# Performance work log

Measured on AMD Instinct MI355X. Metric: run time of the kernel, lower is better.

The kernel has to match this reference:

```python
import jax, jax.numpy as jnp
import numpy as np

B, T, D, U, C = 256, 512, 128, 128, 64


def setup_inputs() -> dict:
    key = jax.random.key(0)
    ks = jax.random.split(key, 4)
    s_in = 1.0 / np.sqrt(D)
    s_u = 1.0 / np.sqrt(U)
    return {
        "inputs": jax.random.normal(ks[0], (B, T, D), dtype=jnp.float32),
        "W1": jax.random.normal(ks[1], (D, U), dtype=jnp.float32) * s_in,
        "b1": jnp.zeros((U,), dtype=jnp.float32),
        "W2": jax.random.normal(ks[2], (U, U), dtype=jnp.float32) * s_u,
        "b2": jnp.zeros((U,), dtype=jnp.float32),
        "Wc": jax.random.normal(ks[3], (U, C), dtype=jnp.float32) * s_u,
        "bc": jnp.zeros((C,), dtype=jnp.float32),
    }


def reference(inputs, W1, b1, W2, b2, Wc, bc):
    # state_{t} = tanh(x_t @ W1 + b1) + tanh(state_{t-1} @ W2 + b2)
    # Input projection has no recurrent dependency -> precompute in one big GEMM.
    h = jnp.tanh(jnp.einsum("btd,du->btu", inputs, W1) + b1)  # (B, T, U)

    def step(state, h_t):
        y = h_t + jnp.tanh(state @ W2 + b2)  # (B, U)
        return y, y

    state0 = jnp.zeros((inputs.shape[0], W2.shape[0]), dtype=inputs.dtype)
    _, ys = jax.lax.scan(step, state0, jnp.swapaxes(h, 0, 1))  # ys: (T, B, U)
    features = jnp.swapaxes(ys, 0, 1)  # (B, T, U)
    # classifier: Dense head applied to stacked features
    return jnp.einsum("btu,uc->btc", features, Wc) + bc
```

## Files before the change

### kernel.cpp

```cpp
#include <hip/hip_runtime.h>

#define NB 256
#define NT 512
#define ND 128
#define NU 128
#define NC 64
#define NM (NB * NT)
#define YP 136
#define SCL 2.8853900817779268f

typedef _Float16 half2v __attribute__((ext_vector_type(2)));
typedef _Float16 half4v __attribute__((ext_vector_type(4)));
typedef _Float16 half8v __attribute__((ext_vector_type(8)));
typedef float f32x4 __attribute__((ext_vector_type(4)));
typedef float v2f __attribute__((ext_vector_type(2)));

#define MFMA(a, b, c) __builtin_amdgcn_mfma_f32_16x16x32_f16((a), (b), (c), 0, 0, 0)

__device__ __forceinline__ half2v pk2(float a, float b) {
  return __builtin_bit_cast(half2v, __builtin_amdgcn_cvt_pkrtz(a, b));
}

__device__ __forceinline__ float tanh_s(float s) {
  float e = __builtin_amdgcn_exp2f(s);
  return fmaf(-2.0f, __builtin_amdgcn_rcpf(e + 1.0f), 1.0f);
}
__device__ __forceinline__ float ytanh(float s, float u) {
  float e = __builtin_amdgcn_exp2f(s);
  return fmaf(-2.0f, __builtin_amdgcn_rcpf(e + 1.0f), u);
}

__device__ __forceinline__ void wg_barrier() {
  asm volatile("s_waitcnt lgkmcnt(0)\n\ts_barrier" ::: "memory");
}

__global__ __launch_bounds__(256, 1) void k1_inproj(
    const float* __restrict__ x, const float* __restrict__ W1,
    const float* __restrict__ b1v, _Float16* __restrict__ TH)
{
  __shared__ _Float16 W1T[ND * YP];
  const int tid = (int)threadIdx.x;
  for (int i = tid; i < ND * NU / 2; i += 256) {
    int n = i & 127, kh = i >> 7;
    half2v p = {(_Float16)(SCL * W1[(size_t)(2 * kh) * NU + n]),
                (_Float16)(SCL * W1[(size_t)(2 * kh + 1) * NU + n])};
    *(half2v*)&W1T[n * YP + 2 * kh] = p;
  }
  __syncthreads();

  const int L = tid & 63, wv = tid >> 6;
  const int v = L & 15, q = L >> 4;
  const int m0 = (int)blockIdx.x * 64 + wv * 16;

  const float* xr = x + (size_t)(m0 + v) * ND + 8 * q;
  half8v xf[4];
#pragma unroll
  for (int kk = 0; kk < 4; ++kk) {
    float4 a = *(const float4*)(xr + 32 * kk);
    float4 b = *(const float4*)(xr + 32 * kk + 4);
    half2v p0 = pk2(a.x, a.y), p1 = pk2(a.z, a.w);
    half2v p2 = pk2(b.x, b.y), p3 = pk2(b.z, b.w);
    xf[kk] = (half8v){p0[0], p0[1], p1[0], p1[1], p2[0], p2[1], p3[0], p3[1]};
  }

#pragma unroll
  for (int ht = 0; ht < 8; ++ht) {
    f32x4 acc;
    {
      float4 bb = *(const float4*)&b1v[16 * ht + 4 * q];
      acc = (f32x4){SCL * bb.x, SCL * bb.y, SCL * bb.z, SCL * bb.w};
    }
#pragma unroll
    for (int kk = 0; kk < 4; ++kk) {
      half8v wa = *(const half8v*)&W1T[(16 * ht + v) * YP + 32 * kk + 8 * q];
      acc = MFMA(wa, xf[kk], acc);
    }
    half2v zlo = pk2(tanh_s(acc[0]), tanh_s(acc[1]));
    half2v zhi = pk2(tanh_s(acc[2]), tanh_s(acc[3]));
    half4v z = {zlo[0], zlo[1], zhi[0], zhi[1]};
    *(half4v*)&TH[(size_t)(m0 + v) * NU + 16 * ht + 4 * q] = z;
  }
}

__global__ __launch_bounds__(512, 1) void k2_recur(
    const _Float16* __restrict__ TH, const float* __restrict__ W2,
    const float* __restrict__ b2v, const float* __restrict__ Wc,
    const float* __restrict__ bcv, float* __restrict__ out)
{
  __shared__ _Float16 Ybuf[2][16 * YP];

  const int tid = (int)threadIdx.x;
  const int w = tid >> 6;
  const int L = tid & 63;
  const int v = L & 15, q = L >> 4;
  const int b0 = (int)blockIdx.x * 16;

  half8v w2f[4];
#pragma unroll
  for (int kk = 0; kk < 4; ++kk) {
    half8v h;
#pragma unroll
    for (int j = 0; j < 8; ++j)
      h[j] = (_Float16)(SCL * W2[(size_t)(32 * kk + 8 * q + j) * NU + 16 * w + v]);
    w2f[kk] = h;
  }
  f32x4 b2f;
  {
    float4 bb = *(const float4*)&b2v[16 * w + 4 * q];
    b2f = (f32x4){SCL * bb.x, SCL * bb.y, SCL * bb.z, SCL * bb.w};
  }

  const bool whead = (w < 4);
  half8v wcf[4];
  f32x4 bcf = (f32x4){0.f, 0.f, 0.f, 0.f};
  float* op = out;
  if (whead) {
#pragma unroll
    for (int kk = 0; kk < 4; ++kk) {
      half8v h;
#pragma unroll
      for (int j = 0; j < 8; ++j)
        h[j] = (_Float16)Wc[(size_t)(32 * kk + 8 * q + j) * NC + 16 * w + v];
      wcf[kk] = h;
    }
    float4 bb = *(const float4*)&bcv[16 * w + 4 * q];
    bcf = (f32x4){bb.x, bb.y, bb.z, bb.w};
    op = out + (size_t)(b0 + v) * NT * NC + 16 * w + 4 * q;
  }

  const _Float16* thp = TH + (size_t)(b0 + v) * NT * NU + 16 * w + 4 * q;

#define CVTU(A)                                                               \
  (f32x4){1.f + (float)(A)[0], 1.f + (float)(A)[1],                           \
          1.f + (float)(A)[2], 1.f + (float)(A)[3]}

  f32x4 uf0, uf1, uf2, uf3;
  {
    half4v a0 = *(const half4v*)(thp + 0 * NU);
    half4v a1 = *(const half4v*)(thp + 1 * NU);
    half4v a2 = *(const half4v*)(thp + 2 * NU);
    half4v a3 = *(const half4v*)(thp + 3 * NU);
    uf0 = CVTU(a0); uf1 = CVTU(a1); uf2 = CVTU(a2); uf3 = CVTU(a3);
  }
  half4v thr0 = *(const half4v*)(thp + 4 * NU);
  half4v thr1 = *(const half4v*)(thp + 5 * NU);
  half4v thr2 = *(const half4v*)(thp + 6 * NU);
  half4v thr3 = *(const half4v*)(thp + 7 * NU);

  f32x4 racc = b2f;
  _Float16* wr = &Ybuf[0][0] + v * YP + 16 * w + 4 * q;
  const _Float16* rd = &Ybuf[0][0] + v * YP + 8 * q;
  const f32x4 zero4 = (f32x4){0.f, 0.f, 0.f, 0.f};

#define K2STEP(T_, UF_, THR_, BUF_)                                           \
  {                                                                           \
    const int t_ = (T_);                                                      \
    half2v ylo = pk2(ytanh(racc[0], UF_[0]), ytanh(racc[1], UF_[1]));         \
    half2v yhi = pk2(ytanh(racc[2], UF_[2]), ytanh(racc[3], UF_[3]));         \
    half4v y4 = {ylo[0], ylo[1], yhi[0], yhi[1]};                             \
    *(half4v*)(wr + (BUF_) * (16 * YP)) = y4;                                 \
    wg_barrier();                                                             \
    half8v yf0 = *(const half8v*)(rd + (BUF_) * (16 * YP) + 0);               \
    half8v yf1 = *(const half8v*)(rd + (BUF_) * (16 * YP) + 32);              \
    half8v yf2 = *(const half8v*)(rd + (BUF_) * (16 * YP) + 64);              \
    half8v yf3 = *(const half8v*)(rd + (BUF_) * (16 * YP) + 96);              \
    f32x4 ra = MFMA(w2f[0], yf0, b2f);          \
    f32x4 rb = MFMA(w2f[1], yf1, zero4);                                      \
    ra = MFMA(w2f[2], yf2, ra);                                               \
    rb = MFMA(w2f[3], yf3, rb);                                               \
    if (whead) {                                                              \
      f32x4 oacc = bcf;                                                       \
      oacc = MFMA(wcf[0], yf0, oacc);                                         \
      oacc = MFMA(wcf[1], yf1, oacc);                                         \
      oacc = MFMA(wcf[2], yf2, oacc);                                         \
      oacc = MFMA(wcf[3], yf3, oacc);                                         \
      *(float4*)(op + (size_t)t_ * NC) =                                      \
          (float4){oacc[0], oacc[1], oacc[2], oacc[3]};                       \
    }                                                                         \
    {                                                                         \
      UF_ = CVTU(THR_);      \
      int tn = t_ + 8; tn = tn < NT ? tn : NT - 1;                            \
      THR_ = *(const half4v*)(thp + (size_t)tn * NU);                         \
    }                                                                         \
    racc = ra + rb;                                                           \
  }

#pragma unroll 1
  for (int t = 0; t < NT; t += 4) {
    K2STEP(t + 0, uf0, thr0, 0)
    K2STEP(t + 1, uf1, thr1, 1)
    K2STEP(t + 2, uf2, thr2, 0)
    K2STEP(t + 3, uf3, thr3, 1)
  }
#undef K2STEP
#undef CVTU
}

__device__ __forceinline__ float fast_tanh(float x) {
  float e = __expf(2.0f * x);
  return 1.0f - 2.0f / (e + 1.0f);
}
__device__ __forceinline__ float bcast(float val, int i) {
  return __builtin_bit_cast(float, __builtin_amdgcn_readlane(__builtin_bit_cast(int, val), i));
}

__global__ __launch_bounds__(256, 1) void rnn_fallback(
    const float* __restrict__ x, const float* __restrict__ W1,
    const float* __restrict__ b1v, const float* __restrict__ W2,
    const float* __restrict__ b2v, const float* __restrict__ Wc,
    const float* __restrict__ bcv, float* __restrict__ out)
{
  __shared__ float xring[16][ND];
  __shared__ float pH[2][4][NU];
  __shared__ float pR[2][4][NU];
  __shared__ float pC[2][4][NC];

  const int tid  = (int)threadIdx.x;
  const int lane = tid & 63;
  const int kg   = tid >> 6;
  const int b    = (int)blockIdx.x;
  const float4* xr4 = (const float4*)(x + (size_t)b * NT * ND);

  v2f w1f[32], w2f[32];
  float wcf[32];
#pragma unroll
  for (int i = 0; i < 32; ++i) {
    int k = kg * 32 + i;
    w1f[i] = (v2f){W1[k * NU + lane], W1[k * NU + lane + 64]};
    w2f[i] = (v2f){W2[k * NU + lane], W2[k * NU + lane + 64]};
    wcf[i] = Wc[k * NC + lane];
  }
  const float biasc = bcv[lane];
  float bias1 = 0.f, bias2 = 0.f;
  if (lane < 32) { bias1 = b1v[kg * 32 + lane]; bias2 = b2v[kg * 32 + lane]; }

  float4 stg = make_float4(0.f, 0.f, 0.f, 0.f);
  if (lane < 32) {
    float4 a0 = xr4[(kg + 0) * 32 + lane];
    float4 a1 = xr4[(kg + 4) * 32 + lane];
    ((float4*)xring[kg + 0])[lane] = a0;
    ((float4*)xring[kg + 4])[lane] = a1;
    stg = xr4[(kg + 8) * 32 + lane];
  }
  float yseg = 0.f;
  wg_barrier();

  for (int t = 0; t < NT; ++t) {
    const int pb = t & 1;
    v2f accH0 = {0.f, 0.f}, accH1 = {0.f, 0.f};
    const float4* xb = (const float4*)&xring[t & 15][kg * 32];
#pragma unroll
    for (int i = 0; i < 4; ++i) {
      float4 xa = xb[2 * i];
      float4 xc = xb[2 * i + 1];
      accH0 = w1f[8*i+0] * (v2f){xa.x, xa.x} + accH0;
      accH1 = w1f[8*i+1] * (v2f){xa.y, xa.y} + accH1;
      accH0 = w1f[8*i+2] * (v2f){xa.z, xa.z} + accH0;
      accH1 = w1f[8*i+3] * (v2f){xa.w, xa.w} + accH1;
      accH0 = w1f[8*i+4] * (v2f){xc.x, xc.x} + accH0;
      accH1 = w1f[8*i+5] * (v2f){xc.y, xc.y} + accH1;
      accH0 = w1f[8*i+6] * (v2f){xc.z, xc.z} + accH0;
      accH1 = w1f[8*i+7] * (v2f){xc.w, xc.w} + accH1;
    }
    v2f accH = accH0 + accH1;
    v2f accR0 = {0.f, 0.f}, accR1 = {0.f, 0.f};
    float accC0 = 0.f, accC1 = 0.f;
#pragma unroll
    for (int i = 0; i < 16; ++i) {
      float s0 = bcast(yseg, 2 * i);
      float s1 = bcast(yseg, 2 * i + 1);
      accR0 = w2f[2*i+0] * (v2f){s0, s0} + accR0;
      accR1 = w2f[2*i+1] * (v2f){s1, s1} + accR1;
      accC0 = fmaf(s0, wcf[2*i+0], accC0);
      accC1 = fmaf(s1, wcf[2*i+1], accC1);
    }
    v2f accR = accR0 + accR1;
    float accC = accC0 + accC1;

    pH[pb][kg][lane]      = accH.x;
    pH[pb][kg][lane + 64] = accH.y;
    pR[pb][kg][lane]      = accR.x;
    pR[pb][kg][lane + 64] = accR.y;
    pC[pb][kg][lane]      = accC;

    if (kg == (t & 3)) {
      if (lane < 32) {
        ((float4*)xring[(t + 8) & 15])[lane] = stg;
        int r = t + 12; r = (r < NT) ? r : (NT - 1);
        stg = xr4[r * 32 + lane];
      }
    }
    wg_barrier();
    if (lane < 32) {
      const int j = kg * 32 + lane;
      float hs = bias1, rs = bias2;
#pragma unroll
      for (int g = 0; g < 4; ++g) { hs += pH[pb][g][j]; rs += pR[pb][g][j]; }
      yseg = fast_tanh(hs) + fast_tanh(rs);
    }
    if (kg == ((t + 2) & 3) && t >= 1) {
      float cs = biasc;
#pragma unroll
      for (int g = 0; g < 4; ++g) cs += pC[pb][g][lane];
      out[((size_t)b * NT + (t - 1)) * NC + lane] = cs;
    }
  }
  float accC0 = 0.f, accC1 = 0.f;
#pragma unroll
  for (int i = 0; i < 16; ++i) {
    float s0 = bcast(yseg, 2 * i);
    float s1 = bcast(yseg, 2 * i + 1);
    accC0 = fmaf(s0, wcf[2*i+0], accC0);
    accC1 = fmaf(s1, wcf[2*i+1], accC1);
  }
  pC[0][kg][lane] = accC0 + accC1;
  wg_barrier();
  if (kg == 0) {
    float cs = biasc;
#pragma unroll
    for (int g = 0; g < 4; ++g) cs += pC[0][g][lane];
    out[((size_t)b * NT + (NT - 1)) * NC + lane] = cs;
  }
}

extern "C" void kernel_launch(void* const* d_in, const int* in_sizes, int n_in,
                              void* d_out, int out_size, void* d_ws, size_t ws_size,
                              hipStream_t stream) {
  (void)in_sizes; (void)n_in; (void)out_size;
  const float* x   = (const float*)d_in[0];
  const float* W1  = (const float*)d_in[1];
  const float* b1v = (const float*)d_in[2];
  const float* W2  = (const float*)d_in[3];
  const float* b2v = (const float*)d_in[4];
  const float* Wc  = (const float*)d_in[5];
  const float* bcv = (const float*)d_in[6];
  float* out = (float*)d_out;

  const size_t need = (size_t)NM * NU * 2;
  if (ws_size >= need) {
    _Float16* TH = (_Float16*)d_ws;
    hipLaunchKernelGGL(k1_inproj, dim3(NM / 64), dim3(256), 0, stream, x, W1, b1v, TH);
    hipLaunchKernelGGL(k2_recur, dim3(NB / 16), dim3(512), 0, stream,
                       TH, W2, b2v, Wc, bcv, out);
  } else {
    hipLaunchKernelGGL(rnn_fallback, dim3(NB), dim3(256), 0, stream,
                       x, W1, b1v, W2, b2v, Wc, bcv, out);
  }
}
```

Measured before the change: 318.5 us.

## Repartition recurrent kernel into two recurrence waves and one dedicated head wave

The recurrent kernel drops from eight waves to three. Two waves each own 64 hidden units and run the W2 recurrence; a third wave computes the whole 64-class classifier head from the shared y buffer. The state is now stored as y minus one, and the column sums of W2 and Wc are folded into the biases, which removes the per-step 1+th conversion. The aim is cheaper per-step workgroup barriers and less idle head work, at the cost of four times more MFMA and tanh work per recurrence wave on the serial critical path.

```diff
diff --git a/kernel.cpp b/kernel.cpp
--- a/kernel.cpp
+++ b/kernel.cpp
@@ -25,9 +25,9 @@
   float e = __builtin_amdgcn_exp2f(s);
   return fmaf(-2.0f, __builtin_amdgcn_rcpf(e + 1.0f), 1.0f);
 }
-__device__ __forceinline__ float ytanh(float s, float u) {
+__device__ __forceinline__ float ym1(float s, float th) {
   float e = __builtin_amdgcn_exp2f(s);
-  return fmaf(-2.0f, __builtin_amdgcn_rcpf(e + 1.0f), u);
+  return fmaf(-2.0f, __builtin_amdgcn_rcpf(e + 1.0f), th);
 }
 
 __device__ __forceinline__ void wg_barrier() {
@@ -82,7 +82,7 @@
   }
 }
 
-__global__ __launch_bounds__(512, 1) void k2_recur(
+__global__ __launch_bounds__(192, 1) void k2_recur(
     const _Float16* __restrict__ TH, const float* __restrict__ W2,
     const float* __restrict__ b2v, const float* __restrict__ Wc,
     const float* __restrict__ bcv, float* __restrict__ out)
@@ -94,106 +94,148 @@
   const int L = tid & 63;
   const int v = L & 15, q = L >> 4;
   const int b0 = (int)blockIdx.x * 16;
-
-  half8v w2f[4];
-#pragma unroll
-  for (int kk = 0; kk < 4; ++kk) {
-    half8v h;
-#pragma unroll
-    for (int j = 0; j < 8; ++j)
-      h[j] = (_Float16)(SCL * W2[(size_t)(32 * kk + 8 * q + j) * NU + 16 * w + v]);
-    w2f[kk] = h;
-  }
-  f32x4 b2f;
-  {
-    float4 bb = *(const float4*)&b2v[16 * w + 4 * q];
-    b2f = (f32x4){SCL * bb.x, SCL * bb.y, SCL * bb.z, SCL * bb.w};
-  }
-
-  const bool whead = (w < 4);
-  half8v wcf[4];
-  f32x4 bcf = (f32x4){0.f, 0.f, 0.f, 0.f};
-  float* op = out;
-  if (whead) {
-#pragma unroll
-    for (int kk = 0; kk < 4; ++kk) {
-      half8v h;
-#pragma unroll
-      for (int j = 0; j < 8; ++j)
-        h[j] = (_Float16)Wc[(size_t)(32 * kk + 8 * q + j) * NC + 16 * w + v];
-      wcf[kk] = h;
-    }
-    float4 bb = *(const float4*)&bcv[16 * w + 4 * q];
-    bcf = (f32x4){bb.x, bb.y, bb.z, bb.w};
-    op = out + (size_t)(b0 + v) * NT * NC + 16 * w + 4 * q;
-  }
-
-  const _Float16* thp = TH + (size_t)(b0 + v) * NT * NU + 16 * w + 4 * q;
-
-#define CVTU(A)                                                               \
-  (f32x4){1.f + (float)(A)[0], 1.f + (float)(A)[1],                           \
-          1.f + (float)(A)[2], 1.f + (float)(A)[3]}
-
-  f32x4 uf0, uf1, uf2, uf3;
-  {
-    half4v a0 = *(const half4v*)(thp + 0 * NU);
-    half4v a1 = *(const half4v*)(thp + 1 * NU);
-    half4v a2 = *(const half4v*)(thp + 2 * NU);
-    half4v a3 = *(const half4v*)(thp + 3 * NU);
-    uf0 = CVTU(a0); uf1 = CVTU(a1); uf2 = CVTU(a2); uf3 = CVTU(a3);
-  }
-  half4v thr0 = *(const half4v*)(thp + 4 * NU);
-  half4v thr1 = *(const half4v*)(thp + 5 * NU);
-  half4v thr2 = *(const half4v*)(thp + 6 * NU);
-  half4v thr3 = *(const half4v*)(thp + 7 * NU);
-
-  f32x4 racc = b2f;
-  _Float16* wr = &Ybuf[0][0] + v * YP + 16 * w + 4 * q;
   const _Float16* rd = &Ybuf[0][0] + v * YP + 8 * q;
   const f32x4 zero4 = (f32x4){0.f, 0.f, 0.f, 0.f};
 
-#define K2STEP(T_, UF_, THR_, BUF_)                                           \
+  if (w < 2) {
+    half8v w2f[4][4];
+#pragma unroll
+    for (int ht = 0; ht < 4; ++ht)
+#pragma unroll
+      for (int kk = 0; kk < 4; ++kk) {
+        half8v h;
+#pragma unroll
+        for (int j = 0; j < 8; ++j)
+          h[j] = (_Float16)(SCL *
+                 W2[(size_t)(32 * kk + 8 * q + j) * NU + 64 * w + 16 * ht + v]);
+        w2f[ht][kk] = h;
+      }
+    f32x4 racc[4], b2f[4];
+#pragma unroll
+    for (int ht = 0; ht < 4; ++ht) {
+      const int h0 = 64 * w + 16 * ht + 4 * q;
+      float4 bb = *(const float4*)&b2v[h0];
+      racc[ht] = (f32x4){SCL * bb.x, SCL * bb.y, SCL * bb.z, SCL * bb.w};
+      f32x4 cs = zero4;
+#pragma unroll 4
+      for (int k = 0; k < NU; ++k) {
+        float4 ww = *(const float4*)&W2[(size_t)k * NU + h0];
+        cs += (f32x4){ww.x, ww.y, ww.z, ww.w};
+      }
+      b2f[ht] = racc[ht] +
+                (f32x4){SCL * cs[0], SCL * cs[1], SCL * cs[2], SCL * cs[3]};
+    }
+
+    const _Float16* thp = TH + ((size_t)(b0 + v) * NT) * NU + 64 * w + 4 * q;
+    _Float16* wr = &Ybuf[0][0] + v * YP + 64 * w + 4 * q;
+
+#define LOADTH(R_, T_)                                                        \
   {                                                                           \
-    const int t_ = (T_);                                                      \
-    half2v ylo = pk2(ytanh(racc[0], UF_[0]), ytanh(racc[1], UF_[1]));         \
-    half2v yhi = pk2(ytanh(racc[2], UF_[2]), ytanh(racc[3], UF_[3]));         \
-    half4v y4 = {ylo[0], ylo[1], yhi[0], yhi[1]};                             \
-    *(half4v*)(wr + (BUF_) * (16 * YP)) = y4;                                 \
+    const _Float16* p_ = thp + (size_t)(T_) * NU;                             \
+    R_[0] = *(const half4v*)(p_);                                             \
+    R_[1] = *(const half4v*)(p_ + 16);                                        \
+    R_[2] = *(const half4v*)(p_ + 32);                                        \
+    R_[3] = *(const half4v*)(p_ + 48);                                        \
+  }
+
+    half4v rg0[4], rg1[4], rg2[4], rg3[4];
+    LOADTH(rg0, 0) LOADTH(rg1, 1) LOADTH(rg2, 2) LOADTH(rg3, 3)
+
+#define RSTEP(T_, R_, BUF_)                                                   \
+  {                                                                           \
+    _Pragma("unroll")                                                         \
+    for (int ht = 0; ht < 4; ++ht) {                                          \
+      half4v t4 = R_[ht];                                                     \
+      half2v ylo = pk2(ym1(racc[ht][0], (float)t4[0]),                        \
+                       ym1(racc[ht][1], (float)t4[1]));                       \
+      half2v yhi = pk2(ym1(racc[ht][2], (float)t4[2]),                        \
+                       ym1(racc[ht][3], (float)t4[3]));                       \
+      half4v y4 = {ylo[0], ylo[1], yhi[0], yhi[1]};                           \
+      *(half4v*)(wr + (BUF_) * (16 * YP) + 16 * ht) = y4;                     \
+    }                                                                         \
+    {                                                                         \
+      int tn = (T_) + 4; tn = tn < NT ? tn : NT - 1;                          \
+      LOADTH(R_, tn)                                                          \
+    }                                                                         \
+    wg_barrier();                                                             \
+    {                                                                         \
+      half8v yf0 = *(const half8v*)(rd + (BUF_) * (16 * YP) + 0);             \
+      half8v yf1 = *(const half8v*)(rd + (BUF_) * (16 * YP) + 32);            \
+      half8v yf2 = *(const half8v*)(rd + (BUF_) * (16 * YP) + 64);            \
+      half8v yf3 = *(const half8v*)(rd + (BUF_) * (16 * YP) + 96);            \
+      _Pragma("unroll")                                                       \
+      for (int ht = 0; ht < 4; ++ht) {                                        \
+        f32x4 ra = MFMA(w2f[ht][0], yf0, b2f[ht]);                            \
+        f32x4 rb = MFMA(w2f[ht][1], yf1, zero4);                              \
+        ra = MFMA(w2f[ht][2], yf2, ra);                                       \
+        rb = MFMA(w2f[ht][3], yf3, rb);                                       \
+        racc[ht] = ra + rb;                                                   \
+      }                                                                       \
+    }                                                                         \
+  }
+
+#pragma unroll 1
+    for (int t = 0; t < NT; t += 4) {
+      RSTEP(t + 0, rg0, 0)
+      RSTEP(t + 1, rg1, 1)
+      RSTEP(t + 2, rg2, 0)
+      RSTEP(t + 3, rg3, 1)
+    }
+#undef RSTEP
+#undef LOADTH
+  } else {
+    half8v wcf[4][4];
+#pragma unroll
+    for (int ct = 0; ct < 4; ++ct)
+#pragma unroll
+      for (int kk = 0; kk < 4; ++kk) {
+        half8v h;
+#pragma unroll
+        for (int j = 0; j < 8; ++j)
+          h[j] = (_Float16)Wc[(size_t)(32 * kk + 8 * q + j) * NC + 16 * ct + v];
+        wcf[ct][kk] = h;
+      }
+    f32x4 bcf[4];
+#pragma unroll
+    for (int ct = 0; ct < 4; ++ct) {
+      const int c0 = 16 * ct + 4 * q;
+      float4 bb = *(const float4*)&bcv[c0];
+      f32x4 cs = zero4;
+#pragma unroll 4
+      for (int k = 0; k < NU; ++k) {
+        float4 ww = *(const float4*)&Wc[(size_t)k * NC + c0];
+        cs += (f32x4){ww.x, ww.y, ww.z, ww.w};
+      }
+      bcf[ct] = cs + (f32x4){bb.x, bb.y, bb.z, bb.w};
+    }
+    float* op = out + ((size_t)(b0 + v) * NT) * NC + 4 * q;
+
+#define HSTEP(T_, BUF_)                                                       \
+  {                                                                           \
     wg_barrier();                                                             \
     half8v yf0 = *(const half8v*)(rd + (BUF_) * (16 * YP) + 0);               \
     half8v yf1 = *(const half8v*)(rd + (BUF_) * (16 * YP) + 32);              \
     half8v yf2 = *(const half8v*)(rd + (BUF_) * (16 * YP) + 64);              \
     half8v yf3 = *(const half8v*)(rd + (BUF_) * (16 * YP) + 96);              \
-    f32x4 ra = MFMA(w2f[0], yf0, b2f);          \
-    f32x4 rb = MFMA(w2f[1], yf1, zero4);                                      \
-    ra = MFMA(w2f[2], yf2, ra);                                               \
-    rb = MFMA(w2f[3], yf3, rb);                                               \
-    if (whead) {                                                              \
-      f32x4 oacc = bcf;                                                       \
-      oacc = MFMA(wcf[0], yf0, oacc);                                         \
-      oacc = MFMA(wcf[1], yf1, oacc);                                         \
-      oacc = MFMA(wcf[2], yf2, oacc);                                         \
-      oacc = MFMA(wcf[3], yf3, oacc);                                         \
-      *(float4*)(op + (size_t)t_ * NC) =                                      \
-          (float4){oacc[0], oacc[1], oacc[2], oacc[3]};                       \
+    _Pragma("unroll")                                                         \
+    for (int ct = 0; ct < 4; ++ct) {                                          \
+      f32x4 oa = MFMA(wcf[ct][0], yf0, bcf[ct]);                              \
+      f32x4 ob = MFMA(wcf[ct][1], yf1, zero4);                                \
+      oa = MFMA(wcf[ct][2], yf2, oa);                                         \
+      ob = MFMA(wcf[ct][3], yf3, ob);                                         \
+      f32x4 oo = oa + ob;                                                     \
+      *(float4*)(op + (size_t)(T_) * NC + 16 * ct) =                          \
+          (float4){oo[0], oo[1], oo[2], oo[3]};                               \
     }                                                                         \
-    {                                                                         \
-      UF_ = CVTU(THR_);      \
-      int tn = t_ + 8; tn = tn < NT ? tn : NT - 1;                            \
-      THR_ = *(const half4v*)(thp + (size_t)tn * NU);                         \
-    }                                                                         \
-    racc = ra + rb;                                                           \
   }
 
 #pragma unroll 1
-  for (int t = 0; t < NT; t += 4) {
-    K2STEP(t + 0, uf0, thr0, 0)
-    K2STEP(t + 1, uf1, thr1, 1)
-    K2STEP(t + 2, uf2, thr2, 0)
-    K2STEP(t + 3, uf3, thr3, 1)
-  }
-#undef K2STEP
-#undef CVTU
+    for (int t = 0; t < NT; t += 2) {
+      HSTEP(t + 0, 0)
+      HSTEP(t + 1, 1)
+    }
+#undef HSTEP
+  }
 }
 
 __device__ __forceinline__ float fast_tanh(float x) {
@@ -340,7 +382,7 @@
   if (ws_size >= need) {
     _Float16* TH = (_Float16*)d_ws;
     hipLaunchKernelGGL(k1_inproj, dim3(NM / 64), dim3(256), 0, stream, x, W1, b1v, TH);
-    hipLaunchKernelGGL(k2_recur, dim3(NB / 16), dim3(512), 0, stream,
+    hipLaunchKernelGGL(k2_recur, dim3(NB / 16), dim3(192), 0, stream,
                        TH, W2, b2v, Wc, bcv, out);
   } else {
     hipLaunchKernelGGL(rnn_fallback, dim3(NB), dim3(256), 0, stream,
```

Measured after the change: 416.4 us. +30.7%, slower.
